# Optimization experiments

Measured on AMD Instinct MI355X. Metric: run time of the kernel, lower is better.

Reference implementation:

```python
import jax, jax.numpy as jnp
from jax import lax
import numpy as np

HEAD_SIZE = 64
D_MIX = 32
D_DECAY = 64
D_GATE = 64


def setup_inputs() -> dict:
    key = jax.random.key(0)
    B, T, C = 4, 2048, 1024
    H = C // HEAD_SIZE
    ks = jax.random.split(key, 24)
    n = lambda i, shape, s=1.0: (jax.random.normal(ks[i], shape, dtype=jnp.float32) * s)
    return {
        "x": n(0, (B, T, C)),
        "maa_x": n(1, (C,), 0.1), "maa_w": n(2, (C,), 0.1), "maa_k": n(3, (C,), 0.1),
        "maa_v": n(4, (C,), 0.1), "maa_r": n(5, (C,), 0.1), "maa_g": n(6, (C,), 0.1),
        "maa_w1": n(7, (C, 5 * D_MIX), 0.01), "maa_w2": n(8, (5, D_MIX, C), 0.01),
        "Wr": n(9, (C, C), C ** -0.5), "Wk": n(10, (C, C), C ** -0.5),
        "Wv": n(11, (C, C), C ** -0.5), "Wo": n(12, (C, C), C ** -0.5),
        "gate_w1": n(13, (C, D_GATE), 0.01), "gate_w2": n(14, (D_GATE, C), 0.01),
        "time_decay": n(15, (C,), 1.0) - 4.0,
        "decay_w1": n(16, (C, D_DECAY), 0.01), "decay_w2": n(17, (D_DECAY, C), 0.01),
        "u": n(18, (H, HEAD_SIZE), 0.1),
        "ln_g": jnp.ones((C,), jnp.float32), "ln_b": jnp.zeros((C,), jnp.float32),
    }


def _wkv6(r, k, v, w, u):
    # r,k,v: [B,T,C]; w: decay (already exp(-exp(.))) [B,T,C]; u: [H,N]
    B, T, C = r.shape
    N = HEAD_SIZE
    H = C // N
    to_h = lambda a: a.reshape(B, T, H, N).transpose(1, 0, 2, 3)  # [T,B,H,N]
    rT, kT, vT, wT = map(to_h, (r, k, v, w))

    def step(S, inp):  # S: [B,H,N,N] (key_dim i x value_dim j)
        rt, kt, vt, wt = inp
        kv = kt[..., :, None] * vt[..., None, :]            # [B,H,N,N]
        y = jnp.einsum('bhi,bhij->bhj', rt, S + u[None, :, :, None] * kv)
        S = wt[..., None] * S + kv
        return S, y

    S0 = jnp.zeros((B, H, N, N), r.dtype)
    _, y = lax.scan(step, S0, (rT, kT, vT, wT))
    return y.transpose(1, 0, 2, 3).reshape(B, T, C)


def reference(x, maa_x, maa_w, maa_k, maa_v, maa_r, maa_g, maa_w1, maa_w2,
              Wr, Wk, Wv, Wo, gate_w1, gate_w2, time_decay, decay_w1, decay_w2,
              u, ln_g, ln_b):
    B, T, C = x.shape
    H, N = C // HEAD_SIZE, HEAD_SIZE
    # time shift: prepend zero row, drop last (ZeroPad2d((0,0,1,-1)))
    xx = jnp.concatenate([jnp.zeros_like(x[:, :1]), x[:, :-1]], axis=1) - x
    xxx = x + xx * maa_x
    lora = jnp.tanh(xxx @ maa_w1).reshape(B, T, 5, D_MIX)
    m = jnp.einsum('btfd,fdc->fbtc', lora, maa_w2)  # [5,B,T,C]
    mw, mk, mv, mr, mg = m[0], m[1], m[2], m[3], m[4]
    xw = x + xx * (maa_w + mw)
    xk = x + xx * (maa_k + mk)
    xv = x + xx * (maa_v + mv)
    xr = x + xx * (maa_r + mr)
    xg = x + xx * (maa_g + mg)
    r = xr @ Wr
    k = xk @ Wk
    v = xv @ Wv
    g = jnp.tanh(xg @ gate_w1) @ gate_w2
    w = time_decay + jnp.tanh(xw @ decay_w1) @ decay_w2
    wdec = jnp.exp(-jnp.exp(w))  # decay applied inside the CUDA kernel
    y = _wkv6(r, k, v, wdec, u)
    # GroupNorm over heads, eps = 1e-5 * HEAD_SIZE_DIVISOR**2 = 6.4e-4
    yh = y.reshape(B, T, H, N)
    mu = yh.mean(-1, keepdims=True)
    var = yh.var(-1, keepdims=True)
    yn = ((yh - mu) / jnp.sqrt(var + 6.4e-4)).reshape(B, T, C) * ln_g + ln_b
    return (yn * g) @ Wo
```

## Files before the change

### kernel.cpp

```cpp
#include <hip/hip_runtime.h>
#include <hip/hip_bf16.h>
#include <stdint.h>

typedef __hip_bfloat16 bf16;
typedef __attribute__((ext_vector_type(8))) short bf16x8;
typedef __attribute__((ext_vector_type(4))) float f32x4;

#define CC 1024
#define TT 2048
#define BB 4
#define BT 8192
#define HH 16
#define NN 64

#define MFMA(a, b, c) __builtin_amdgcn_mfma_f32_16x16x32_bf16(a, b, c, 0, 0, 0)

#define GLD(g, l) __builtin_amdgcn_global_load_lds( \
    (const __attribute__((address_space(1))) void*)(g), \
    (__attribute__((address_space(3))) void*)(l), 16, 0, 0)

__device__ __forceinline__ short f2bs(float f) {
    bf16 h = __float2bfloat16(f);
    return *reinterpret_cast<short*>(&h);
}
__device__ __forceinline__ float bs2f(short s) {
    bf16 h = *reinterpret_cast<bf16*>(&s);
    return __bfloat162float(h);
}

template <typename EPI>
__device__ __forceinline__ void gemm128(short* As, short* Bs,
                                        const bf16* __restrict__ A, int lda,
                                        const bf16* __restrict__ Bt, int ldb,
                                        int kiters, int m0, int n0, EPI epi)
{
    const int tid = threadIdx.x;
    const int l   = tid & 63, wv = tid >> 6;
    const int wm  = wv >> 1, wn = wv & 1;
    const int q   = l >> 4, lr = l & 15;
    const int row = tid & 127, kg1 = tid >> 7;

    f32x4 acc[4][4] = {};

    const bf16* ga = A  + (size_t)(m0 + row) * lda + kg1 * 8;
    const bf16* gb = Bt + (size_t)(n0 + row) * ldb + kg1 * 8;
    short* la1 = As + tid * 8;
    short* la2 = As + (tid + 256) * 8;
    short* lb1 = Bs + tid * 8;
    short* lb2 = Bs + (tid + 256) * 8;

    for (int kb = 0; kb < kiters; ++kb) {
        __syncthreads();
        const bf16* gak = ga + kb * 32;
        const bf16* gbk = gb + kb * 32;
        GLD(gak,      la1);
        GLD(gak + 16, la2);
        GLD(gbk,      lb1);
        GLD(gbk + 16, lb2);
        __syncthreads();
        bf16x8 af[4], bfb[4];
#pragma unroll
        for (int mt = 0; mt < 4; ++mt)
            af[mt] = *(const bf16x8*)(As + (q * 128 + wm * 64 + mt * 16 + lr) * 8);
#pragma unroll
        for (int nt = 0; nt < 4; ++nt)
            bfb[nt] = *(const bf16x8*)(Bs + (q * 128 + wn * 64 + nt * 16 + lr) * 8);
#pragma unroll
        for (int mt = 0; mt < 4; ++mt)
#pragma unroll
            for (int nt = 0; nt < 4; ++nt)
                acc[mt][nt] = MFMA(af[mt], bfb[nt], acc[mt][nt]);
    }
#pragma unroll
    for (int mt = 0; mt < 4; ++mt)
#pragma unroll
        for (int nt = 0; nt < 4; ++nt)
#pragma unroll
            for (int rr = 0; rr < 4; ++rr)
                epi(m0 + wm * 64 + mt * 16 + q * 4 + rr,
                    n0 + wn * 64 + nt * 16 + lr, acc[mt][nt][rr]);
}

template <typename EPI>
__device__ __forceinline__ void gemm128k64(short* As, short* Bs,
                                           const bf16* __restrict__ A, int lda,
                                           const bf16* __restrict__ Bt, int ldb,
                                           int kiters, int m0, int n0, EPI epi)
{
    const int tid = threadIdx.x;
    const int l   = tid & 63, wv = tid >> 6;
    const int wm  = wv >> 1, wn = wv & 1;
    const int q   = l >> 4, lr = l & 15;
    const int row = tid & 127, kg1 = tid >> 7;

    f32x4 acc[4][4] = {};

    const bf16* ga = A  + (size_t)(m0 + row) * lda + kg1 * 8;
    const bf16* gb = Bt + (size_t)(n0 + row) * ldb + kg1 * 8;

    auto stage = [&](int kb, int u) {
        const bf16* gak = ga + kb * 64;
        const bf16* gbk = gb + kb * 64;
        short* la = As + u * 8192 + tid * 8;
        short* lb = Bs + u * 8192 + tid * 8;
        GLD(gak,      la);
        GLD(gak + 16, la + 2048);
        GLD(gak + 32, la + 4096);
        GLD(gak + 48, la + 6144);
        GLD(gbk,      lb);
        GLD(gbk + 16, lb + 2048);
        GLD(gbk + 32, lb + 4096);
        GLD(gbk + 48, lb + 6144);
    };

    __syncthreads();
    stage(0, 0);
    __syncthreads();
    for (int kb = 0; kb < kiters; ++kb) {
        const int cur = kb & 1;
        if (kb + 1 < kiters) stage(kb + 1, cur ^ 1);
        const short* Ac = As + cur * 8192;
        const short* Bc = Bs + cur * 8192;
        bf16x8 af[2][4], bfb[2][4];
#pragma unroll
        for (int hh = 0; hh < 2; ++hh) {
#pragma unroll
            for (int mt = 0; mt < 4; ++mt)
                af[hh][mt] = *(const bf16x8*)(Ac +
                    ((q + hh * 4) * 128 + wm * 64 + mt * 16 + lr) * 8);
#pragma unroll
            for (int nt = 0; nt < 4; ++nt)
                bfb[hh][nt] = *(const bf16x8*)(Bc +
                    ((q + hh * 4) * 128 + wn * 64 + nt * 16 + lr) * 8);
        }
        __builtin_amdgcn_s_setprio(1);
#pragma unroll
        for (int mt = 0; mt < 4; ++mt)
#pragma unroll
            for (int nt = 0; nt < 4; ++nt) {
                acc[mt][nt] = MFMA(af[0][mt], bfb[0][nt], acc[mt][nt]);
                acc[mt][nt] = MFMA(af[1][mt], bfb[1][nt], acc[mt][nt]);
            }
        __builtin_amdgcn_s_setprio(0);
        __syncthreads();
    }
#pragma unroll
    for (int mt = 0; mt < 4; ++mt)
#pragma unroll
        for (int nt = 0; nt < 4; ++nt)
#pragma unroll
            for (int rr = 0; rr < 4; ++rr)
                epi(m0 + wm * 64 + mt * 16 + q * 4 + rr,
                    n0 + wn * 64 + nt * 16 + lr, acc[mt][nt][rr]);
}

__global__ __launch_bounds__(256) void k_prep_all(
    const float* __restrict__ Wr, const float* __restrict__ Wk,
    const float* __restrict__ Wv, const float* __restrict__ Wo,
    const float* __restrict__ maa_w1, const float* __restrict__ gate_w1,
    const float* __restrict__ decay_w1, const float* __restrict__ gate_w2,
    const float* __restrict__ decay_w2, const float* __restrict__ maa_w2,
    const float* __restrict__ mw, const float* __restrict__ mk,
    const float* __restrict__ mv, const float* __restrict__ mr,
    const float* __restrict__ mg, const float* __restrict__ x,
    const float* __restrict__ maa_x,
    bf16* __restrict__ WT3, bf16* __restrict__ WoT, bf16* __restrict__ w1T,
    bf16* __restrict__ w1T2, bf16* __restrict__ w2T2, bf16* __restrict__ w2T5,
    float* __restrict__ maas, bf16* __restrict__ xxx,
    bf16* __restrict__ xb, bf16* __restrict__ xxb)
{
    __shared__ float tile[32][33];
    int idx = blockIdx.x;
    if (idx >= 4900) {
        size_t i = ((size_t)(idx - 4900) * 256 + threadIdx.x) * 4;
        int cc = i & (CC - 1);
        int t  = (i >> 10) & (TT - 1);
        float4 xm = *(const float4*)(x + i);
        float4 xp = t ? *(const float4*)(x + i - CC)
                      : make_float4(0.f, 0.f, 0.f, 0.f);
        float4 ax = *(const float4*)(maa_x + cc);
        float xxv[4] = {xp.x - xm.x, xp.y - xm.y, xp.z - xm.z, xp.w - xm.w};
        float xmv[4] = {xm.x, xm.y, xm.z, xm.w};
        float axv[4] = {ax.x, ax.y, ax.z, ax.w};
#pragma unroll
        for (int e = 0; e < 4; ++e) {
            xb[i + e]  = __float2bfloat16(xmv[e]);
            xxb[i + e] = __float2bfloat16(xxv[e]);
            xxx[i + e] = __float2bfloat16(xmv[e] + xxv[e] * axv[e]);
        }
        return;
    }
    const float* src; bf16* dst; int rows, cols_in, tx_;
    if (idx < 4096) {
        int s = idx >> 10; idx &= 1023;
        src = (s == 0) ? Wr : (s == 1) ? Wk : (s == 2) ? Wv : Wo;
        dst = (s == 3) ? WoT : WT3 + (size_t)s * CC * CC;
        rows = CC; cols_in = CC; tx_ = 32;
    } else if (idx < 4352) { idx -= 4096; src = maa_w1;  dst = w1T;  rows = CC; cols_in = 160; tx_ = 8; }
    else if (idx < 4480)   { idx -= 4352; src = gate_w1; dst = w1T2; rows = CC; cols_in = 64;  tx_ = 4; }
    else if (idx < 4608)   { idx -= 4480; src = decay_w1; dst = w1T2 + 128 * CC; rows = CC; cols_in = 64; tx_ = 4; }
    else if (idx < 4672)   { idx -= 4608; src = gate_w2;  dst = w2T2;           rows = 64; cols_in = CC; tx_ = 32; }
    else if (idx < 4736)   { idx -= 4672; src = decay_w2; dst = w2T2 + CC * 64; rows = 64; cols_in = CC; tx_ = 32; }
    else if (idx < 4896)   { idx -= 4736; int f = idx >> 5; idx &= 31;
                             src = maa_w2 + (size_t)f * 32 * CC;
                             dst = w2T5 + (size_t)f * CC * 32; rows = 32; cols_in = CC; tx_ = 32; }
    else {
        int i = (idx - 4896) * 256 + threadIdx.x;
        if (i < CC) {
            maas[i]          = mw[i];
            maas[CC + i]     = mk[i];
            maas[2 * CC + i] = mv[i];
            maas[3 * CC + i] = mr[i];
            maas[4 * CC + i] = mg[i];
        }
        return;
    }
    int bx = idx % tx_, by = idx / tx_;
    int c0 = bx * 32, r0 = by * 32;
    int tx = threadIdx.x & 31, ty = threadIdx.x >> 5;
    for (int i = ty; i < 32; i += 8) {
        int cc2 = c0 + tx;
        tile[i][tx] = (cc2 < cols_in) ? src[(size_t)(r0 + i) * cols_in + cc2] : 0.f;
    }
    __syncthreads();
    for (int i = ty; i < 32; i += 8)
        dst[(size_t)(c0 + i) * rows + r0 + tx] = __float2bfloat16(tile[tx][i]);
}

__global__ __launch_bounds__(256) void g_lora(const bf16* __restrict__ xxx,
                                              const bf16* __restrict__ w1T,
                                              bf16* __restrict__ L)
{
    __shared__ __align__(16) short lds[8192];
    int m0 = blockIdx.x * 128, n0 = blockIdx.y * 128;
    gemm128(lds, lds + 4096, xxx, CC, w1T, CC, CC / 32, m0, n0,
            [&](int m, int n, float v) {
                if (n < 160) L[(size_t)m * 160 + n] = __float2bfloat16(tanhf(v));
            });
}

__global__ __launch_bounds__(256) void g_xvar(const bf16* __restrict__ L,
                                              const bf16* __restrict__ w2T,
                                              const float* __restrict__ maas,
                                              const bf16* __restrict__ xb,
                                              const bf16* __restrict__ xxb,
                                              bf16* __restrict__ xvars)
{
    __shared__ __align__(16) short lds[8192];
    int m0 = blockIdx.x * 128, n0 = blockIdx.y * 128;
    for (int f = 0; f < 5; ++f) {
        const bf16* A  = L + f * 32;
        const bf16* Bt = w2T + (size_t)f * CC * 32;
        const float* maa = maas + f * CC;
        bf16* out = xvars + (size_t)f * BT * CC;
        gemm128(lds, lds + 4096, A, 160, Bt, 32, 1, m0, n0,
                [&](int m, int n, float v) {
                    float xm = __bfloat162float(xb[(size_t)m * CC + n]);
                    float xx = __bfloat162float(xxb[(size_t)m * CC + n]);
                    out[(size_t)m * CC + n] =
                        __float2bfloat16(xm + xx * (maa[n] + v));
                });
    }
}

__global__ __launch_bounds__(256) void g_rkv5(const bf16* __restrict__ xvars,
                                              const bf16* __restrict__ WT,
                                              const bf16* __restrict__ w1T2,
                                              bf16* __restrict__ rkv,
                                              bf16* __restrict__ hid)
{
    __shared__ __align__(16) short lds[32768];
    int z = blockIdx.z;
    int m0 = blockIdx.x * 128;
    if (blockIdx.y < 8) {
        int n0 = blockIdx.y * 128;
        int f = (z == 0) ? 3 : z;
        const bf16* A  = xvars + (size_t)f * BT * CC;
        const bf16* Bt = WT + (size_t)z * CC * CC;
        bf16* out = rkv + (size_t)z * BT * CC;
        gemm128k64(lds, lds + 16384, A, CC, Bt, CC, CC / 64, m0, n0,
                   [&](int m, int n, float v) {
                       out[(size_t)m * CC + n] = __float2bfloat16(v);
                   });
    } else {
        if (z == 2) return;
        int zz = z;
        const bf16* A  = xvars + (size_t)(zz == 0 ? 4 : 0) * BT * CC;
        const bf16* Bt = w1T2 + (size_t)zz * 128 * CC;
        bf16* out = hid + (size_t)zz * BT * 64;
        gemm128k64(lds, lds + 16384, A, CC, Bt, CC, CC / 64, m0, 0,
                   [&](int m, int n, float v) {
                       if (n < 64) out[(size_t)m * 64 + n] = __float2bfloat16(tanhf(v));
                   });
    }
}

__global__ __launch_bounds__(256) void k_wkv_p1(const bf16* __restrict__ r,
                                                const bf16* __restrict__ kk,
                                                const bf16* __restrict__ vv,
                                                const bf16* __restrict__ hidW,
                                                const bf16* __restrict__ w2d,
                                                const float* __restrict__ td,
                                                const float* __restrict__ u,
                                                bf16* __restrict__ y,
                                                bf16* __restrict__ RTg,
                                                short* __restrict__ Mg,
                                                float* __restrict__ plg)
{
    constexpr int PW = 65, PB = 72;
    __shared__ __align__(16) char smem[16640 + 3 * 9216 + 768];
    float* LW = (float*)smem;
    short* VT = (short*)smem;
    short* RT = (short*)(smem + 16640);
    short* KT = (short*)(smem + 16640 + 9216);
    short* AT = KT;
    short* KH = (short*)(smem + 16640 + 2 * 9216);
    short* HT = KT;
    short* WD = KH;
    float* SU = (float*)(smem + 16640 + 3 * 9216);
    float* SD = SU + 64;

    const int tid = threadIdx.x;
    const int lane = tid & 63, wq = tid >> 6;
    const int row = tid >> 2, g = tid & 3, j0 = g * 16;
    const int l15 = lane & 15, q = lane >> 4;
    const int bh = blockIdx.x >> 5, c = blockIdx.x & 31;
    const int b = bh >> 4, h = bh & 15;
    const size_t base = (size_t)b * TT * CC + (size_t)h * NN;
    const int t0 = c * 64;
    const int bt0 = b * TT + t0;
    const size_t cb = (size_t)blockIdx.x * 4096;

    if (tid < 64) SU[tid] = u[h * NN + tid];

#pragma unroll
    for (int rnd = 0; rnd < 2; ++rnd) {
        int ee = rnd * 256 + tid;
        int rw = ee >> 3, c8 = (ee & 7) * 8;
        *(bf16x8*)(HT + rw * PB + c8) =
            *(const bf16x8*)(hidW + (size_t)(bt0 + rw) * 64 + c8);
        *(bf16x8*)(WD + rw * PB + c8) =
            *(const bf16x8*)(w2d + (size_t)(h * 64 + rw) * 64 + c8);
    }
    const size_t gb = base + (size_t)(t0 + row) * CC + j0;
    bf16x8 r0 = *(const bf16x8*)(r + gb),  r1 = *(const bf16x8*)(r + gb + 8);
    bf16x8 k0 = *(const bf16x8*)(kk + gb), k1 = *(const bf16x8*)(kk + gb + 8);
    bf16x8 v0 = *(const bf16x8*)(vv + gb), v1 = *(const bf16x8*)(vv + gb + 8);
    float tdv[4];
#pragma unroll
    for (int ct = 0; ct < 4; ++ct) tdv[ct] = td[h * 64 + ct * 16 + l15];
    __syncthreads();
    {
        bf16x8 aH0 = *(const bf16x8*)(HT + (wq * 16 + l15) * PB + q * 8);
        bf16x8 aH1 = *(const bf16x8*)(HT + (wq * 16 + l15) * PB + q * 8 + 32);
        f32x4 lwa[4] = {};
#pragma unroll
        for (int ct = 0; ct < 4; ++ct) {
            bf16x8 bW0 = *(const bf16x8*)(WD + (ct * 16 + l15) * PB + q * 8);
            bf16x8 bW1 = *(const bf16x8*)(WD + (ct * 16 + l15) * PB + q * 8 + 32);
            lwa[ct] = MFMA(aH0, bW0, lwa[ct]);
            lwa[ct] = MFMA(aH1, bW1, lwa[ct]);
        }
#pragma unroll
        for (int ct = 0; ct < 4; ++ct)
#pragma unroll
            for (int rr = 0; rr < 4; ++rr) {
                int t = wq * 16 + q * 4 + rr, j = ct * 16 + l15;
                LW[t * PW + j] = -expf(tdv[ct] + lwa[ct][rr]);
            }
    }
    __syncthreads();
    for (int jj = 0; jj < 16; ++jj) {
        int j = wq * 16 + jj;
        float xv = LW[lane * PW + j];
#pragma unroll
        for (int d = 1; d < 64; d <<= 1) {
            float t2 = __shfl_up(xv, d);
            if (lane >= d) xv += t2;
        }
        LW[lane * PW + j] = xv;
    }
    __syncthreads();
    float rF[16], kF[16];
#pragma unroll
    for (int c2 = 0; c2 < 8; ++c2) {
        rF[c2] = bs2f(r0[c2]); rF[8 + c2] = bs2f(r1[c2]);
        kF[c2] = bs2f(k0[c2]); kF[8 + c2] = bs2f(k1[c2]);
    }
    float cwp[16], cwm[16], cwL[16];
#pragma unroll
    for (int c2 = 0; c2 < 16; ++c2) {
        cwp[c2] = LW[row * PW + j0 + c2];
        cwm[c2] = row ? LW[(row - 1) * PW + j0 + c2] : 0.f;
        cwL[c2] = LW[63 * PW + j0 + c2];
    }
    bf16x8 w0, w1;
#pragma unroll
    for (int c2 = 0; c2 < 8; ++c2) {
        w0[c2] = f2bs(rF[c2] * expf(cwm[c2]));
        w1[c2] = f2bs(rF[8 + c2] * expf(cwm[8 + c2]));
    }
    *(bf16x8*)(RT + row * PB + j0)     = w0;
    *(bf16x8*)(RT + row * PB + j0 + 8) = w1;
    *(bf16x8*)((short*)RTg + cb + row * 64 + j0)     = w0;
    *(bf16x8*)((short*)RTg + cb + row * 64 + j0 + 8) = w1;
#pragma unroll
    for (int c2 = 0; c2 < 8; ++c2) {
        w0[c2] = f2bs(kF[c2] * expf(-cwp[c2]));
        w1[c2] = f2bs(kF[8 + c2] * expf(-cwp[8 + c2]));
    }
    *(bf16x8*)(KT + row * PB + j0)     = w0;
    *(bf16x8*)(KT + row * PB + j0 + 8) = w1;
#pragma unroll
    for (int c2 = 0; c2 < 16; ++c2)
        KH[(j0 + c2) * PB + row] = f2bs(kF[c2] * expf(cwL[c2] - cwp[c2]));
    if (tid < 64) plg[(size_t)blockIdx.x * 64 + tid] = expf(LW[63 * PW + tid]);
    float dpart = 0.f;
#pragma unroll
    for (int c2 = 0; c2 < 16; ++c2)
        dpart = fmaf(rF[c2] * kF[c2], SU[j0 + c2], dpart);
    dpart += __shfl_xor(dpart, 1);
    dpart += __shfl_xor(dpart, 2);
    if (g == 0) SD[row] = dpart;
    __syncthreads();
#pragma unroll
    for (int c2 = 0; c2 < 8; ++c2) {
        VT[(j0 + c2) * PB + row]     = v0[c2];
        VT[(j0 + 8 + c2) * PB + row] = v1[c2];
    }
    bf16x8 aF0 = *(const bf16x8*)(RT + (wq * 16 + l15) * PB + q * 8);
    bf16x8 aF1 = *(const bf16x8*)(RT + (wq * 16 + l15) * PB + q * 8 + 32);
    f32x4 Am[4] = {};
#pragma unroll
    for (int ct = 0; ct < 4; ++ct) {
        bf16x8 bF0 = *(const bf16x8*)(KT + (ct * 16 + l15) * PB + q * 8);
        bf16x8 bF1 = *(const bf16x8*)(KT + (ct * 16 + l15) * PB + q * 8 + 32);
        Am[ct] = MFMA(aF0, bF0, Am[ct]);
        Am[ct] = MFMA(aF1, bF1, Am[ct]);
    }
    __syncthreads();
#pragma unroll
    for (int ct = 0; ct < 4; ++ct)
#pragma unroll
        for (int rr = 0; rr < 4; ++rr) {
            int s = wq * 16 + q * 4 + rr, p = ct * 16 + l15;
            float vA = Am[ct][rr];
            vA = (p > s) ? 0.f : (p == s ? SD[s] : vA);
            AT[s * PB + p] = f2bs(vA);
        }
    __syncthreads();
    f32x4 Y[4] = {}, M[4] = {};
    bf16x8 aA0 = *(const bf16x8*)(AT + (wq * 16 + l15) * PB + q * 8);
    bf16x8 aA1 = *(const bf16x8*)(AT + (wq * 16 + l15) * PB + q * 8 + 32);
    bf16x8 aV0 = *(const bf16x8*)(VT + (wq * 16 + l15) * PB + q * 8);
    bf16x8 aV1 = *(const bf16x8*)(VT + (wq * 16 + l15) * PB + q * 8 + 32);
#pragma unroll
    for (int ct = 0; ct < 4; ++ct) {
        bf16x8 bV0 = *(const bf16x8*)(VT + (ct * 16 + l15) * PB + q * 8);
        bf16x8 bV1 = *(const bf16x8*)(VT + (ct * 16 + l15) * PB + q * 8 + 32);
        Y[ct] = MFMA(aA0, bV0, Y[ct]);
        Y[ct] = MFMA(aA1, bV1, Y[ct]);
        bf16x8 bK0 = *(const bf16x8*)(KH + (ct * 16 + l15) * PB + q * 8);
        bf16x8 bK1 = *(const bf16x8*)(KH + (ct * 16 + l15) * PB + q * 8 + 32);
        M[ct] = MFMA(aV0, bK0, M[ct]);
        M[ct] = MFMA(aV1, bK1, M[ct]);
    }
#pragma unroll
    for (int ct = 0; ct < 4; ++ct)
#pragma unroll
        for (int rr = 0; rr < 4; ++rr) {
            int s = wq * 16 + q * 4 + rr;
            y[base + (size_t)(t0 + s) * CC + ct * 16 + l15] =
                __float2bfloat16(Y[ct][rr]);
            Mg[cb + (size_t)s * 64 + ct * 16 + l15] = f2bs(M[ct][rr]);
        }
}

__global__ __launch_bounds__(256) void k_wkv_p2(const short* __restrict__ Mg,
                                                const float* __restrict__ plg,
                                                bf16* __restrict__ Sg)
{
    int bh = blockIdx.x >> 4, part = blockIdx.x & 15;
    int i = part * 4 + (threadIdx.x >> 6), j = threadIdx.x & 63;
    float S = 0.f;
    size_t eb = (size_t)bh * 32 * 4096 + (size_t)i * 64 + j;
    size_t pb = (size_t)bh * 32 * 64 + j;
    for (int c = 0; c < 32; ++c) {
        Sg[eb + (size_t)c * 4096] = __float2bfloat16(S);
        S = plg[pb + (size_t)c * 64] * S + bs2f(Mg[eb + (size_t)c * 4096]);
    }
}

__global__ __launch_bounds__(256) void k_wkv_p3(const bf16* __restrict__ RTg,
                                                const bf16* __restrict__ Sg,
                                                const bf16* __restrict__ y,
                                                const bf16* __restrict__ hidG,
                                                const bf16* __restrict__ w2g,
                                                const float* __restrict__ ln_g,
                                                const float* __restrict__ ln_b,
                                                bf16* __restrict__ A2)
{
    constexpr int PB = 72;
    __shared__ __align__(16) short BufA[64 * PB], BufB[64 * PB];
    const int tid = threadIdx.x;
    const int lane = tid & 63, wq = tid >> 6;
    const int l15 = lane & 15, q = lane >> 4;
    const int bh = blockIdx.x >> 5, c = blockIdx.x & 31;
    const int b = bh >> 4, h = bh & 15;
    const int t0 = c * 64;
    const int bt0 = b * TT + t0;
    const size_t cb = (size_t)blockIdx.x * 4096;

#pragma unroll
    for (int rnd = 0; rnd < 2; ++rnd) {
        int ee = rnd * 256 + tid;
        int rw = ee >> 3, c8 = (ee & 7) * 8;
        *(bf16x8*)(BufA + rw * PB + c8) =
            *(const bf16x8*)(hidG + (size_t)(bt0 + rw) * 64 + c8);
        *(bf16x8*)(BufB + rw * PB + c8) =
            *(const bf16x8*)(w2g + (size_t)(h * 64 + rw) * 64 + c8);
    }
    __syncthreads();
    f32x4 G[4] = {};
    {
        bf16x8 aH0 = *(const bf16x8*)(BufA + (wq * 16 + l15) * PB + q * 8);
        bf16x8 aH1 = *(const bf16x8*)(BufA + (wq * 16 + l15) * PB + q * 8 + 32);
#pragma unroll
        for (int ct = 0; ct < 4; ++ct) {
            bf16x8 bW0 = *(const bf16x8*)(BufB + (ct * 16 + l15) * PB + q * 8);
            bf16x8 bW1 = *(const bf16x8*)(BufB + (ct * 16 + l15) * PB + q * 8 + 32);
            G[ct] = MFMA(aH0, bW0, G[ct]);
            G[ct] = MFMA(aH1, bW1, G[ct]);
        }
    }
    __syncthreads();
#pragma unroll
    for (int rnd = 0; rnd < 2; ++rnd) {
        int ee = rnd * 256 + tid;
        int rw = ee >> 3, c8 = (ee & 7) * 8;
        *(bf16x8*)(BufA + rw * PB + c8) =
            *(const bf16x8*)((const short*)RTg + cb + rw * 64 + c8);
        *(bf16x8*)(BufB + rw * PB + c8) =
            *(const bf16x8*)((const short*)Sg + cb + rw * 64 + c8);
    }
    __syncthreads();

    f32x4 Yc[4];
#pragma unroll
    for (int ct = 0; ct < 4; ++ct)
#pragma unroll
        for (int rr = 0; rr < 4; ++rr) {
            int s = wq * 16 + q * 4 + rr;
            Yc[ct][rr] = __bfloat162float(
                y[((size_t)bt0 + s) * CC + h * NN + ct * 16 + l15]);
        }
    bf16x8 aF0 = *(const bf16x8*)(BufA + (wq * 16 + l15) * PB + q * 8);
    bf16x8 aF1 = *(const bf16x8*)(BufA + (wq * 16 + l15) * PB + q * 8 + 32);
#pragma unroll
    for (int ct = 0; ct < 4; ++ct) {
        bf16x8 bS0 = *(const bf16x8*)(BufB + (ct * 16 + l15) * PB + q * 8);
        bf16x8 bS1 = *(const bf16x8*)(BufB + (ct * 16 + l15) * PB + q * 8 + 32);
        Yc[ct] = MFMA(aF0, bS0, Yc[ct]);
        Yc[ct] = MFMA(aF1, bS1, Yc[ct]);
    }
#pragma unroll
    for (int rr = 0; rr < 4; ++rr) {
        float s1 = 0.f, s2 = 0.f;
#pragma unroll
        for (int ct = 0; ct < 4; ++ct) {
            float vA = Yc[ct][rr];
            s1 += vA; s2 += vA * vA;
        }
#pragma unroll
        for (int o = 1; o < 16; o <<= 1) {
            s1 += __shfl_xor(s1, o);
            s2 += __shfl_xor(s2, o);
        }
        float mu  = s1 * (1.f / 64.f);
        float var = s2 * (1.f / 64.f) - mu * mu;
        float rstd = rsqrtf(var + 6.4e-4f);
        int s = wq * 16 + q * 4 + rr;
        size_t mrow = ((size_t)bt0 + s) * CC;
#pragma unroll
        for (int ct = 0; ct < 4; ++ct) {
            int ch = h * NN + ct * 16 + l15;
            float yn = (Yc[ct][rr] - mu) * rstd;
            float out = (yn * ln_g[ch] + ln_b[ch]) * G[ct][rr];
            A2[mrow + ch] = __float2bfloat16(out);
        }
    }
}

__global__ __launch_bounds__(256) void g_out(const bf16* __restrict__ A2,
                                             const bf16* __restrict__ WoT,
                                             float* __restrict__ out)
{
    __shared__ __align__(16) short lds[32768];
    int m0 = blockIdx.x * 128, n0 = blockIdx.y * 128;
    gemm128k64(lds, lds + 16384, A2, CC, WoT, CC, CC / 64, m0, n0,
               [&](int m, int n, float v) { out[(size_t)m * CC + n] = v; });
}

extern "C" void kernel_launch(void* const* d_in, const int* in_sizes, int n_in,
                              void* d_out, int out_size, void* d_ws, size_t ws_size,
                              hipStream_t stream)
{
    const float* x        = (const float*)d_in[0];
    const float* maa_x    = (const float*)d_in[1];
    const float* maa_w    = (const float*)d_in[2];
    const float* maa_k    = (const float*)d_in[3];
    const float* maa_v    = (const float*)d_in[4];
    const float* maa_r    = (const float*)d_in[5];
    const float* maa_g    = (const float*)d_in[6];
    const float* maa_w1   = (const float*)d_in[7];
    const float* maa_w2   = (const float*)d_in[8];
    const float* Wr       = (const float*)d_in[9];
    const float* Wk       = (const float*)d_in[10];
    const float* Wv       = (const float*)d_in[11];
    const float* Wo       = (const float*)d_in[12];
    const float* gate_w1  = (const float*)d_in[13];
    const float* gate_w2  = (const float*)d_in[14];
    const float* time_dec = (const float*)d_in[15];
    const float* decay_w1 = (const float*)d_in[16];
    const float* decay_w2 = (const float*)d_in[17];
    const float* u        = (const float*)d_in[18];
    const float* ln_g     = (const float*)d_in[19];
    const float* ln_b     = (const float*)d_in[20];

    size_t off = 0;
    auto alloc = [&](size_t bytes) {
        off = (off + 255) & ~(size_t)255;
        void* p = (char*)d_ws + off;
        off += bytes;
        return p;
    };
    bf16*  WT3   = (bf16*) alloc(3ull * CC * CC * 2);
    bf16*  WoT   = (bf16*) alloc((size_t)CC * CC * 2);
    bf16*  w1T   = (bf16*) alloc(256ull * CC * 2);
    bf16*  w1T2  = (bf16*) alloc(2ull * 128 * CC * 2);
    bf16*  w2T2  = (bf16*) alloc(2ull * CC * 64 * 2);
    bf16*  w2T5  = (bf16*) alloc(5ull * CC * 32 * 2);
    float* maas  = (float*)alloc(5ull * CC * 4);
    char* bufA = (char*)alloc((size_t)BT * CC * 2);
    bf16* xxxbf = (bf16*)bufA;
    bf16* A2    = (bf16*)bufA;
    char* bufB = (char*)alloc((size_t)BT * 160 * 2);
    bf16* Lbf  = (bf16*)bufB;
    bf16* hid  = (bf16*)bufB;
    char* bufC = (char*)alloc(5ull * BT * CC * 2);
    bf16*  xvars = (bf16*)bufC;
    bf16*  ybuf  = (bf16*)bufC;
    bf16*  RTg   = (bf16*)(bufC + (size_t)BT * CC * 2);
    bf16*  rkv  = (bf16*)alloc(3ull * BT * CC * 2);
    bf16*  Sg   = rkv;
    bf16*  xb   = (bf16*) alloc((size_t)BT * CC * 2);
    bf16*  xxb  = (bf16*) alloc((size_t)BT * CC * 2);
    short* Mg   = (short*)alloc(64ull * 32 * 4096 * 2);
    float* plg  = (float*)alloc(64ull * 32 * 64 * 4);

    k_prep_all<<<dim3(13092), 256, 0, stream>>>(
        Wr, Wk, Wv, Wo, maa_w1, gate_w1, decay_w1, gate_w2, decay_w2, maa_w2,
        maa_w, maa_k, maa_v, maa_r, maa_g, x, maa_x,
        WT3, WoT, w1T, w1T2, w2T2, w2T5, maas, xxxbf, xb, xxb);

    g_lora<<<dim3(64, 2), 256, 0, stream>>>(xxxbf, w1T, Lbf);
    g_xvar<<<dim3(64, 8), 256, 0, stream>>>(Lbf, w2T5, maas, xb, xxb, xvars);
    g_rkv5<<<dim3(64, 9, 3), 256, 0, stream>>>(xvars, WT3, w1T2, rkv, hid);
    k_wkv_p1<<<dim3(2048), 256, 0, stream>>>(rkv, rkv + (size_t)BT * CC,
                                             rkv + 2ull * BT * CC,
                                             hid + (size_t)BT * 64,
                                             w2T2 + CC * 64,
                                             time_dec, u, ybuf, RTg, Mg, plg);
    k_wkv_p2<<<dim3(1024), 256, 0, stream>>>(Mg, plg, Sg);
    k_wkv_p3<<<dim3(2048), 256, 0, stream>>>(RTg, Sg, ybuf,
                                             hid,
                                             w2T2,
                                             ln_g, ln_b, A2);
    g_out<<<dim3(64, 8), 256, 0, stream>>>(A2, WoT, (float*)d_out);
}
```

Baseline: 417.8 us.

## Use 256x256 tiles with 512 threads and a dedicated hidden GEMM in g_rkv5

Replaces the 128x128 GEMM tiles in the r/k/v projection kernel with 256x256 tiles computed by 512-thread blocks, roughly doubling the arithmetic done per byte loaded into LDS. The launch becomes a flat 1D grid with a swizzled block order meant to improve L2 reuse of the weight tiles. The low-rank gate and decay projections move to a specialised 256x64 GEMM, so they no longer compute a padded 128-wide N tile or launch idle z==2 blocks. The cost is 128 KB of LDS per block and higher register pressure from 32 accumulators per thread, which limits occupancy to one block per CU.

```diff
diff --git a/kernel.cpp b/kernel.cpp
--- a/kernel.cpp
+++ b/kernel.cpp
@@ -152,6 +152,143 @@
             for (int rr = 0; rr < 4; ++rr)
                 epi(m0 + wm * 64 + mt * 16 + q * 4 + rr,
                     n0 + wn * 64 + nt * 16 + lr, acc[mt][nt][rr]);
+}
+
+template <typename EPI>
+__device__ __forceinline__ void gemm256(short* As, short* Bs,
+                                        const bf16* __restrict__ A, int lda,
+                                        const bf16* __restrict__ Bt, int ldb,
+                                        int kiters, int m0, int n0, EPI epi)
+{
+    const int tid = threadIdx.x;
+    const int l   = tid & 63, wv = tid >> 6;
+    const int wm  = wv >> 2, wn = wv & 3;
+    const int q   = l >> 4, lr = l & 15;
+    const int row = tid & 255, kg = tid >> 8;
+
+    f32x4 acc[8][4] = {};
+
+    const bf16* ga = A  + (size_t)(m0 + row) * lda + kg * 8;
+    const bf16* gb = Bt + (size_t)(n0 + row) * ldb + kg * 8;
+
+    auto stage = [&](int kb, int u) {
+        const bf16* gak = ga + kb * 64;
+        const bf16* gbk = gb + kb * 64;
+        short* la = As + u * 16384 + tid * 8;
+        short* lb = Bs + u * 16384 + tid * 8;
+        GLD(gak,      la);
+        GLD(gak + 16, la + 4096);
+        GLD(gak + 32, la + 8192);
+        GLD(gak + 48, la + 12288);
+        GLD(gbk,      lb);
+        GLD(gbk + 16, lb + 4096);
+        GLD(gbk + 32, lb + 8192);
+        GLD(gbk + 48, lb + 12288);
+    };
+
+    __syncthreads();
+    stage(0, 0);
+    __syncthreads();
+    for (int kb = 0; kb < kiters; ++kb) {
+        const int cur = kb & 1;
+        if (kb + 1 < kiters) stage(kb + 1, cur ^ 1);
+        const short* Ac = As + cur * 16384;
+        const short* Bc = Bs + cur * 16384;
+#pragma unroll
+        for (int hh = 0; hh < 2; ++hh) {
+            bf16x8 af[8], bfb[4];
+#pragma unroll
+            for (int mt = 0; mt < 8; ++mt)
+                af[mt] = *(const bf16x8*)(Ac +
+                    ((q + hh * 4) * 256 + wm * 128 + mt * 16 + lr) * 8);
+#pragma unroll
+            for (int nt = 0; nt < 4; ++nt)
+                bfb[nt] = *(const bf16x8*)(Bc +
+                    ((q + hh * 4) * 256 + wn * 64 + nt * 16 + lr) * 8);
+            __builtin_amdgcn_s_setprio(1);
+#pragma unroll
+            for (int mt = 0; mt < 8; ++mt)
+#pragma unroll
+                for (int nt = 0; nt < 4; ++nt)
+                    acc[mt][nt] = MFMA(af[mt], bfb[nt], acc[mt][nt]);
+            __builtin_amdgcn_s_setprio(0);
+        }
+        __syncthreads();
+    }
+#pragma unroll
+    for (int mt = 0; mt < 8; ++mt)
+#pragma unroll
+        for (int nt = 0; nt < 4; ++nt)
+#pragma unroll
+            for (int rr = 0; rr < 4; ++rr)
+                epi(m0 + wm * 128 + mt * 16 + q * 4 + rr,
+                    n0 + wn * 64 + nt * 16 + lr, acc[mt][nt][rr]);
+}
+
+template <typename EPI>
+__device__ __forceinline__ void gemmHid(short* As, short* Bs,
+                                        const bf16* __restrict__ A, int lda,
+                                        const bf16* __restrict__ Bt, int ldb,
+                                        int kiters, int m0, EPI epi)
+{
+    const int tid = threadIdx.x;
+    const int l   = tid & 63, wv = tid >> 6;
+    const int q   = l >> 4, lr = l & 15;
+    const int row = tid & 255, kg = tid >> 8;
+    const int row64 = tid & 63, kg8 = tid >> 6;
+
+    f32x4 acc[2][4] = {};
+
+    const bf16* ga = A  + (size_t)(m0 + row) * lda + kg * 8;
+    const bf16* gb = Bt + (size_t)row64 * ldb + kg8 * 8;
+
+    auto stage = [&](int kb, int u) {
+        const bf16* gak = ga + kb * 64;
+        short* la = As + u * 16384 + tid * 8;
+        GLD(gak,      la);
+        GLD(gak + 16, la + 4096);
+        GLD(gak + 32, la + 8192);
+        GLD(gak + 48, la + 12288);
+        GLD(gb + kb * 64, Bs + u * 4096 + tid * 8);
+    };
+
+    __syncthreads();
+    stage(0, 0);
+    __syncthreads();
+    for (int kb = 0; kb < kiters; ++kb) {
+        const int cur = kb & 1;
+        if (kb + 1 < kiters) stage(kb + 1, cur ^ 1);
+        const short* Ac = As + cur * 16384;
+        const short* Bc = Bs + cur * 4096;
+        bf16x8 af[2][2], bfb[2][4];
+#pragma unroll
+        for (int hh = 0; hh < 2; ++hh) {
+#pragma unroll
+            for (int mt = 0; mt < 2; ++mt)
+                af[hh][mt] = *(const bf16x8*)(Ac +
+                    ((q + hh * 4) * 256 + wv * 32 + mt * 16 + lr) * 8);
+#pragma unroll
+            for (int nt = 0; nt < 4; ++nt)
+                bfb[hh][nt] = *(const bf16x8*)(Bc +
+                    ((q + hh * 4) * 64 + nt * 16 + lr) * 8);
+        }
+#pragma unroll
+        for (int mt = 0; mt < 2; ++mt)
+#pragma unroll
+            for (int nt = 0; nt < 4; ++nt) {
+                acc[mt][nt] = MFMA(af[0][mt], bfb[0][nt], acc[mt][nt]);
+                acc[mt][nt] = MFMA(af[1][mt], bfb[1][nt], acc[mt][nt]);
+            }
+        __syncthreads();
+    }
+#pragma unroll
+    for (int mt = 0; mt < 2; ++mt)
+#pragma unroll
+        for (int nt = 0; nt < 4; ++nt)
+#pragma unroll
+            for (int rr = 0; rr < 4; ++rr)
+                epi(m0 + wv * 32 + mt * 16 + q * 4 + rr,
+                    nt * 16 + lr, acc[mt][nt][rr]);
 }
 
 __global__ __launch_bounds__(256) void k_prep_all(
@@ -263,35 +400,38 @@
     }
 }
 
-__global__ __launch_bounds__(256) void g_rkv5(const bf16* __restrict__ xvars,
+__global__ __launch_bounds__(512) void g_rkv5(const bf16* __restrict__ xvars,
                                               const bf16* __restrict__ WT,
                                               const bf16* __restrict__ w1T2,
                                               bf16* __restrict__ rkv,
                                               bf16* __restrict__ hid)
 {
-    __shared__ __align__(16) short lds[32768];
-    int z = blockIdx.z;
-    int m0 = blockIdx.x * 128;
-    if (blockIdx.y < 8) {
-        int n0 = blockIdx.y * 128;
+    __shared__ __align__(16) short lds[65536];
+    int bid = blockIdx.x;
+    if (bid < 384) {
+        int swz = (bid & 7) * 48 + (bid >> 3);
+        int z  = swz >> 7;
+        int r2 = swz & 127;
+        int n0 = (r2 >> 5) * 256;
+        int m0 = (r2 & 31) * 256;
         int f = (z == 0) ? 3 : z;
         const bf16* A  = xvars + (size_t)f * BT * CC;
         const bf16* Bt = WT + (size_t)z * CC * CC;
         bf16* out = rkv + (size_t)z * BT * CC;
-        gemm128k64(lds, lds + 16384, A, CC, Bt, CC, CC / 64, m0, n0,
-                   [&](int m, int n, float v) {
-                       out[(size_t)m * CC + n] = __float2bfloat16(v);
-                   });
+        gemm256(lds, lds + 32768, A, CC, Bt, CC, CC / 64, m0, n0,
+                [&](int m, int n, float v) {
+                    out[(size_t)m * CC + n] = __float2bfloat16(v);
+                });
     } else {
-        if (z == 2) return;
-        int zz = z;
+        int hb = bid - 384;
+        int zz = hb >> 5, mi = hb & 31;
         const bf16* A  = xvars + (size_t)(zz == 0 ? 4 : 0) * BT * CC;
         const bf16* Bt = w1T2 + (size_t)zz * 128 * CC;
         bf16* out = hid + (size_t)zz * BT * 64;
-        gemm128k64(lds, lds + 16384, A, CC, Bt, CC, CC / 64, m0, 0,
-                   [&](int m, int n, float v) {
-                       if (n < 64) out[(size_t)m * 64 + n] = __float2bfloat16(tanhf(v));
-                   });
+        gemmHid(lds, lds + 32768, A, CC, Bt, CC, CC / 64, mi * 256,
+                [&](int m, int n, float v) {
+                    out[(size_t)m * 64 + n] = __float2bfloat16(tanhf(v));
+                });
     }
 }
 
@@ -665,7 +805,7 @@
 
     g_lora<<<dim3(64, 2), 256, 0, stream>>>(xxxbf, w1T, Lbf);
     g_xvar<<<dim3(64, 8), 256, 0, stream>>>(Lbf, w2T5, maas, xb, xxb, xvars);
-    g_rkv5<<<dim3(64, 9, 3), 256, 0, stream>>>(xvars, WT3, w1T2, rkv, hid);
+    g_rkv5<<<dim3(448), 512, 0, stream>>>(xvars, WT3, w1T2, rkv, hid);
     k_wkv_p1<<<dim3(2048), 256, 0, stream>>>(rkv, rkv + (size_t)BT * CC,
                                              rkv + 2ull * BT * CC,
                                              hid + (size_t)BT * 64,
```

Result: faster. 401.9 us (-3.8%).
